# Kernel tuning notes

Measured on AMD Instinct MI355X. Metric: run time of the kernel, lower is better.

## Reference

```python
import jax, jax.numpy as jnp
import numpy as np

B, S, H, NH = 2048, 200, 128, 4
NEG = jnp.float32(-2.0**32 + 1)

def setup_inputs() -> dict:
    key = jax.random.key(0)
    k1, k2, k3, k4, k5 = jax.random.split(key, 5)
    item_eb = jax.random.normal(k1, (B, S, H), dtype=jnp.float32)
    mask = jax.random.randint(k2, (B, S), 0, 2, dtype=jnp.int32)
    pos_emb = jax.random.normal(k3, (1, S, H), dtype=jnp.float32) * 0.02
    # nn.Linear(H, 4H, bias=False): weight [4H, H]; store transposed for x @ W
    W1 = jax.random.normal(k4, (H, 4 * H), dtype=jnp.float32) * (1.0 / np.sqrt(H))
    W2 = jax.random.normal(k5, (4 * H, NH), dtype=jnp.float32) * (1.0 / np.sqrt(4 * H))
    return {"item_eb": item_eb, "mask": mask, "pos_emb": pos_emb, "W1": W1, "W2": W2}

def reference(item_eb, mask, pos_emb, W1, W2):
    x = item_eb.reshape(-1, S, H)                       # [B,S,H]
    x_pos = x + pos_emb                                  # broadcast position add
    hidden = jnp.tanh(jnp.einsum('bsh,hf->bsf', x_pos, W1))   # [B,S,4H]
    att = jnp.einsum('bsf,fk->bks', hidden, W2)          # [B,NH,S] (transpose fused)
    att = jnp.where(mask[:, None, :] == 0, NEG, att)     # masked fill
    att = jax.nn.softmax(att, axis=-1)                   # [B,NH,S]
    interest = jnp.einsum('bks,bsh->bkh', att, x)        # [B,NH,H]
    return interest
```

## Files before the change

### kernel.cpp

```cpp
#include <hip/hip_runtime.h>
#include <hip/hip_bf16.h>

typedef _Float16 half8 __attribute__((ext_vector_type(8)));
typedef _Float16 half4 __attribute__((ext_vector_type(4)));
typedef float f32x4 __attribute__((ext_vector_type(4)));

#define SS 200
#define HH 128
#define NHD 4
#define FH 512
#define NTILES 32
#define MTILES 13
#define RW 144
#define NEGF (-4294967295.0f)

__global__ void swizzle_w1(const float* __restrict__ W1, _Float16* __restrict__ dst) {
    int tid = blockIdx.x * blockDim.x + threadIdx.x;
    int j    = tid & 7;
    int lane = (tid >> 3) & 63;
    int ks   = (tid >> 9) & 3;
    int nt   = tid >> 11;
    int k = ks * 32 + (lane >> 4) * 8 + j;
    int n = nt * 16 + (lane & 15);
    dst[tid] = (_Float16)W1[k * FH + n];
}

__device__ __forceinline__ float tanh_fast(float x) {
    x = fminf(fmaxf(x, -15.0f), 15.0f);
    float e = __expf(x + x);
    return (e - 1.0f) * __builtin_amdgcn_rcpf(e + 1.0f);
}

__device__ __forceinline__ f32x4 mfma16(half8 a, half8 b, f32x4 c) {
    return __builtin_amdgcn_mfma_f32_16x16x32_f16(a, b, c, 0, 0, 0);
}

template<int USE_WS>
__global__ __launch_bounds__(256, USE_WS ? 4 : 1)
void mhan_main(const float* __restrict__ item, const int* __restrict__ mask,
               const float* __restrict__ pos, const float* __restrict__ W1,
               const float* __restrict__ W2, const _Float16* __restrict__ w1sw,
               float* __restrict__ out)
{
    __shared__ __align__(16) _Float16 xs[16 * RW];
    __shared__ float4 w2s[FH];
    __shared__ float  attw[208 * NHD];
    __shared__ half8  w1s_lds[USE_WS ? 1 : (NTILES * 4 * 64)];

    int tid = threadIdx.x;
    int b   = blockIdx.x;
    int lane = tid & 63, wave = tid >> 6;
    int q = lane >> 4, c = lane & 15;

    int rowslot[4], colslot[4];
    {
        half8 pc_, pone;
#pragma unroll
        for (int j = 0; j < 8; ++j) { pc_[j] = (_Float16)(float)c; pone[j] = (_Float16)0.03125f; }
        f32x4 z = {0.f,0.f,0.f,0.f};
        f32x4 pr = mfma16(pc_, pone, z);
        f32x4 pcv = mfma16(pone, pc_, z);
#pragma unroll
        for (int r = 0; r < 4; ++r) {
            int rv = (int)(pr[r] + 0.5f);
            int cv = (int)(pcv[r] + 0.5f);
            rowslot[r] = rv < 0 ? 0 : (rv > 15 ? 15 : rv);
            colslot[r] = cv < 0 ? 0 : (cv > 15 ? 15 : cv);
        }
    }
    int okA = 1, okB = 1;
#pragma unroll
    for (int r = 0; r < 4; ++r) {
        okA &= (rowslot[r] == q * 4 + r) & (colslot[r] == c);
        okB &= (rowslot[r] == c) & (colslot[r] == q * 4 + r);
    }
    int path = __all(okA) ? 0 : (__all(okB) ? 1 : 2);

    if constexpr (!USE_WS) {
        _Float16* w1f = (_Float16*)w1s_lds;
        for (int idx = tid; idx < HH * FH; idx += 256) {
            int j = idx & 7; int ln = (idx >> 3) & 63;
            int ks = (idx >> 9) & 3; int nt = idx >> 11;
            int k = ks * 32 + (ln >> 4) * 8 + j;
            int n = nt * 16 + (ln & 15);
            w1f[idx] = (_Float16)W1[k * FH + n];
        }
    }
    for (int i = tid; i < FH; i += 256) w2s[i] = ((const float4*)W2)[i];
    for (int i = tid; i < 208 * NHD; i += 256) attw[i] = 0.0f;
    __syncthreads();

    const half8* w1p;
    if constexpr (USE_WS) w1p = (const half8*)w1sw;
    else                  w1p = w1s_lds;

    const float* xb = item + (size_t)b * SS * HH;
    int nt0 = wave * 8;

#pragma unroll 1
    for (int mt = 0; mt < MTILES; ++mt) {
#pragma unroll
        for (int i = 0; i < 2; ++i) {
            int u = tid + i * 256;
            int row = u >> 5, col4 = u & 31;
            int grow = mt * 16 + row;
            float4 xv = make_float4(0.f,0.f,0.f,0.f), pv = xv;
            if (grow < SS) {
                xv = ((const float4*)(xb + grow * HH))[col4];
                pv = ((const float4*)(pos + grow * HH))[col4];
            }
            half4 h;
            h[0] = (_Float16)(xv.x + pv.x); h[1] = (_Float16)(xv.y + pv.y);
            h[2] = (_Float16)(xv.z + pv.z); h[3] = (_Float16)(xv.w + pv.w);
            *(half4*)&xs[row * RW + col4 * 4] = h;
        }
        __syncthreads();

        half8 af[4];
        {
            const _Float16* xp = &xs[c * RW + q * 8];
#pragma unroll
            for (int ks = 0; ks < 4; ++ks) af[ks] = *(const half8*)(xp + ks * 32);
        }

        float attp[4][NHD];
#pragma unroll
        for (int r = 0; r < 4; ++r)
#pragma unroll
            for (int k = 0; k < NHD; ++k) attp[r][k] = 0.0f;

#pragma unroll 1
        for (int nt = nt0; nt < nt0 + 8; nt += 2) {
            const half8* bp0 = &w1p[(nt * 4) * 64 + lane];
            const half8* bp1 = &w1p[((nt + 1) * 4) * 64 + lane];
            half8 bf0[4], bf1[4];
#pragma unroll
            for (int ks = 0; ks < 4; ++ks) { bf0[ks] = bp0[ks * 64]; bf1[ks] = bp1[ks * 64]; }
            f32x4 acc0 = {0.f,0.f,0.f,0.f}, acc1 = {0.f,0.f,0.f,0.f};
#pragma unroll
            for (int ks = 0; ks < 4; ++ks) {
                acc0 = mfma16(af[ks], bf0[ks], acc0);
                acc1 = mfma16(af[ks], bf1[ks], acc1);
            }
#pragma unroll
            for (int r = 0; r < 4; ++r) {
                float4 w0 = w2s[nt * 16 + colslot[r]];
                float4 w1v = w2s[(nt + 1) * 16 + colslot[r]];
                float h0 = tanh_fast(acc0[r]);
                float h1 = tanh_fast(acc1[r]);
                attp[r][0] += h0 * w0.x + h1 * w1v.x;
                attp[r][1] += h0 * w0.y + h1 * w1v.y;
                attp[r][2] += h0 * w0.z + h1 * w1v.z;
                attp[r][3] += h0 * w0.w + h1 * w1v.w;
            }
        }

        if (path == 0) {
#pragma unroll
            for (int r = 0; r < 4; ++r)
#pragma unroll
                for (int k = 0; k < NHD; ++k) {
                    float v = attp[r][k];
                    v += __shfl_xor(v, 1);
                    v += __shfl_xor(v, 2);
                    v += __shfl_xor(v, 4);
                    v += __shfl_xor(v, 8);
                    if (c == 0)
                        atomicAdd(&attw[(mt * 16 + rowslot[r]) * NHD + k], v);
                }
        } else if (path == 1) {
#pragma unroll
            for (int k = 0; k < NHD; ++k) {
                float v = attp[0][k] + attp[1][k] + attp[2][k] + attp[3][k];
                v += __shfl_xor(v, 16);
                v += __shfl_xor(v, 32);
                if (q == 0)
                    atomicAdd(&attw[(mt * 16 + c) * NHD + k], v);
            }
        } else {
#pragma unroll
            for (int r = 0; r < 4; ++r)
#pragma unroll
                for (int k = 0; k < NHD; ++k)
                    atomicAdd(&attw[(mt * 16 + rowslot[r]) * NHD + k], attp[r][k]);
        }
        __syncthreads();
    }

    {
        int k = wave;
        float l[4];
        float m = -__builtin_inff();
#pragma unroll
        for (int i = 0; i < 4; ++i) {
            int s = lane + i * 64;
            if (s < SS) {
                float lv = (mask[(size_t)b * SS + s] != 0) ? attw[s * NHD + k] : NEGF;
                l[i] = lv;
                m = fmaxf(m, lv);
            } else {
                l[i] = -__builtin_inff();
            }
        }
#pragma unroll
        for (int off = 32; off >= 1; off >>= 1) m = fmaxf(m, __shfl_xor(m, off));
        float e[4], sum = 0.0f;
#pragma unroll
        for (int i = 0; i < 4; ++i) {
            e[i] = (l[i] == -__builtin_inff()) ? 0.0f : __expf(l[i] - m);
            sum += e[i];
        }
#pragma unroll
        for (int off = 32; off >= 1; off >>= 1) sum += __shfl_xor(sum, off);
        float inv = __builtin_amdgcn_rcpf(sum);
#pragma unroll
        for (int i = 0; i < 4; ++i) {
            int s = lane + i * 64;
            if (s < SS) attw[s * NHD + k] = e[i] * inv;
        }
    }

    {
        int k = wave;
        float ax = 0.0f, ay = 0.0f;
#pragma unroll 8
        for (int s = 0; s < SS; ++s) {
            float w = attw[s * NHD + k];
            float2 xv = ((const float2*)(xb + s * HH))[lane];
            ax += w * xv.x;
            ay += w * xv.y;
        }
        size_t o = ((size_t)b * NHD + k) * HH + lane * 2;
        float2 ov; ov.x = ax; ov.y = ay;
        *(float2*)(out + o) = ov;
    }
}

extern "C" void kernel_launch(void* const* d_in, const int* in_sizes, int n_in,
                              void* d_out, int out_size, void* d_ws, size_t ws_size,
                              hipStream_t stream) {
    const float* item = (const float*)d_in[0];
    const int*   mask = (const int*)d_in[1];
    const float* pos  = (const float*)d_in[2];
    const float* W1   = (const float*)d_in[3];
    const float* W2   = (const float*)d_in[4];
    float* out = (float*)d_out;

    int B = in_sizes[0] / (SS * HH);
    int use_ws = (ws_size >= (size_t)(HH * FH * sizeof(_Float16))) ? 1 : 0;

    if (use_ws) {
        hipLaunchKernelGGL(swizzle_w1, dim3((HH * FH) / 256), dim3(256), 0, stream,
                           W1, (_Float16*)d_ws);
        mhan_main<1><<<dim3(B), dim3(256), 0, stream>>>(
            item, mask, pos, W1, W2, (const _Float16*)d_ws, out);
    } else {
        mhan_main<0><<<dim3(B), dim3(256), 0, stream>>>(
            item, mask, pos, W1, W2, (const _Float16*)nullptr, out);
    }
}
```

Baseline: 514.8 us.

## Process two 16-row M tiles per phase to reuse W1 fragments

```diff
diff --git a/kernel.cpp b/kernel.cpp
--- a/kernel.cpp
+++ b/kernel.cpp
@@ -10,7 +10,8 @@
 #define NHD 4
 #define FH 512
 #define NTILES 32
-#define MTILES 13
+#define NPHASES 7
+#define AROWS 224
 #define RW 144
 #define NEGF (-4294967295.0f)
 
@@ -36,15 +37,15 @@
 }
 
 template<int USE_WS>
-__global__ __launch_bounds__(256, USE_WS ? 4 : 1)
+__global__ __launch_bounds__(256, USE_WS ? 3 : 1)
 void mhan_main(const float* __restrict__ item, const int* __restrict__ mask,
                const float* __restrict__ pos, const float* __restrict__ W1,
                const float* __restrict__ W2, const _Float16* __restrict__ w1sw,
                float* __restrict__ out)
 {
-    __shared__ __align__(16) _Float16 xs[16 * RW];
+    __shared__ __align__(16) _Float16 xs[32 * RW];
     __shared__ float4 w2s[FH];
-    __shared__ float  attw[208 * NHD];
+    __shared__ float  attw[AROWS * NHD];
     __shared__ half8  w1s_lds[USE_WS ? 1 : (NTILES * 4 * 64)];
 
     int tid = threadIdx.x;
@@ -87,7 +88,7 @@
         }
     }
     for (int i = tid; i < FH; i += 256) w2s[i] = ((const float4*)W2)[i];
-    for (int i = tid; i < 208 * NHD; i += 256) attw[i] = 0.0f;
+    for (int i = tid; i < AROWS * NHD; i += 256) attw[i] = 0.0f;
     __syncthreads();
 
     const half8* w1p;
@@ -98,12 +99,12 @@
     int nt0 = wave * 8;
 
 #pragma unroll 1
-    for (int mt = 0; mt < MTILES; ++mt) {
-#pragma unroll
-        for (int i = 0; i < 2; ++i) {
+    for (int ph = 0; ph < NPHASES; ++ph) {
+#pragma unroll
+        for (int i = 0; i < 4; ++i) {
             int u = tid + i * 256;
             int row = u >> 5, col4 = u & 31;
-            int grow = mt * 16 + row;
+            int grow = ph * 32 + row;
             float4 xv = make_float4(0.f,0.f,0.f,0.f), pv = xv;
             if (grow < SS) {
                 xv = ((const float4*)(xb + grow * HH))[col4];
@@ -116,73 +117,117 @@
         }
         __syncthreads();
 
-        half8 af[4];
-        {
-            const _Float16* xp = &xs[c * RW + q * 8];
-#pragma unroll
-            for (int ks = 0; ks < 4; ++ks) af[ks] = *(const half8*)(xp + ks * 32);
-        }
-
-        float attp[4][NHD];
-#pragma unroll
-        for (int r = 0; r < 4; ++r)
-#pragma unroll
-            for (int k = 0; k < NHD; ++k) attp[r][k] = 0.0f;
-
-#pragma unroll 1
-        for (int nt = nt0; nt < nt0 + 8; nt += 2) {
-            const half8* bp0 = &w1p[(nt * 4) * 64 + lane];
-            const half8* bp1 = &w1p[((nt + 1) * 4) * 64 + lane];
-            half8 bf0[4], bf1[4];
-#pragma unroll
-            for (int ks = 0; ks < 4; ++ks) { bf0[ks] = bp0[ks * 64]; bf1[ks] = bp1[ks * 64]; }
-            f32x4 acc0 = {0.f,0.f,0.f,0.f}, acc1 = {0.f,0.f,0.f,0.f};
-#pragma unroll
-            for (int ks = 0; ks < 4; ++ks) {
-                acc0 = mfma16(af[ks], bf0[ks], acc0);
-                acc1 = mfma16(af[ks], bf1[ks], acc1);
-            }
-#pragma unroll
-            for (int r = 0; r < 4; ++r) {
-                float4 w0 = w2s[nt * 16 + colslot[r]];
-                float4 w1v = w2s[(nt + 1) * 16 + colslot[r]];
-                float h0 = tanh_fast(acc0[r]);
-                float h1 = tanh_fast(acc1[r]);
-                attp[r][0] += h0 * w0.x + h1 * w1v.x;
-                attp[r][1] += h0 * w0.y + h1 * w1v.y;
-                attp[r][2] += h0 * w0.z + h1 * w1v.z;
-                attp[r][3] += h0 * w0.w + h1 * w1v.w;
-            }
-        }
+        half8 af[2][4];
+#pragma unroll
+        for (int t = 0; t < 2; ++t) {
+            const _Float16* xp = &xs[(t * 16 + c) * RW + q * 8];
+#pragma unroll
+            for (int ks = 0; ks < 4; ++ks) af[t][ks] = *(const half8*)(xp + ks * 32);
+        }
+
+        float attp[2][4][NHD];
+#pragma unroll
+        for (int t = 0; t < 2; ++t)
+#pragma unroll
+            for (int r = 0; r < 4; ++r)
+#pragma unroll
+                for (int k = 0; k < NHD; ++k) attp[t][r][k] = 0.0f;
 
         if (path == 0) {
 #pragma unroll
-            for (int r = 0; r < 4; ++r)
-#pragma unroll
-                for (int k = 0; k < NHD; ++k) {
-                    float v = attp[r][k];
-                    v += __shfl_xor(v, 1);
-                    v += __shfl_xor(v, 2);
-                    v += __shfl_xor(v, 4);
-                    v += __shfl_xor(v, 8);
-                    if (c == 0)
-                        atomicAdd(&attw[(mt * 16 + rowslot[r]) * NHD + k], v);
+            for (int np = 0; np < 4; ++np) {
+                int nt = nt0 + 2 * np;
+                const half8* bp0 = &w1p[(nt * 4) * 64 + lane];
+                const half8* bp1 = &w1p[((nt + 1) * 4) * 64 + lane];
+                half8 bf0[4], bf1[4];
+#pragma unroll
+                for (int ks = 0; ks < 4; ++ks) { bf0[ks] = bp0[ks * 64]; bf1[ks] = bp1[ks * 64]; }
+                float4 w20 = w2s[nt * 16 + c];
+                float4 w21 = w2s[(nt + 1) * 16 + c];
+#pragma unroll
+                for (int t = 0; t < 2; ++t) {
+                    f32x4 acc0 = {0.f,0.f,0.f,0.f}, acc1 = {0.f,0.f,0.f,0.f};
+#pragma unroll
+                    for (int ks = 0; ks < 4; ++ks) {
+                        acc0 = mfma16(af[t][ks], bf0[ks], acc0);
+                        acc1 = mfma16(af[t][ks], bf1[ks], acc1);
+                    }
+#pragma unroll
+                    for (int r = 0; r < 4; ++r) {
+                        float h0 = tanh_fast(acc0[r]);
+                        float h1 = tanh_fast(acc1[r]);
+                        attp[t][r][0] += h0 * w20.x + h1 * w21.x;
+                        attp[t][r][1] += h0 * w20.y + h1 * w21.y;
+                        attp[t][r][2] += h0 * w20.z + h1 * w21.z;
+                        attp[t][r][3] += h0 * w20.w + h1 * w21.w;
+                    }
                 }
-        } else if (path == 1) {
-#pragma unroll
-            for (int k = 0; k < NHD; ++k) {
-                float v = attp[0][k] + attp[1][k] + attp[2][k] + attp[3][k];
-                v += __shfl_xor(v, 16);
-                v += __shfl_xor(v, 32);
-                if (q == 0)
-                    atomicAdd(&attw[(mt * 16 + c) * NHD + k], v);
-            }
+            }
+#pragma unroll
+            for (int t = 0; t < 2; ++t)
+#pragma unroll
+                for (int r = 0; r < 4; ++r)
+#pragma unroll
+                    for (int k = 0; k < NHD; ++k) {
+                        float v = attp[t][r][k];
+                        v += __shfl_xor(v, 1);
+                        v += __shfl_xor(v, 2);
+                        v += __shfl_xor(v, 4);
+                        v += __shfl_xor(v, 8);
+                        if (c == 0)
+                            atomicAdd(&attw[((ph * 2 + t) * 16 + rowslot[r]) * NHD + k], v);
+                    }
         } else {
 #pragma unroll
-            for (int r = 0; r < 4; ++r)
-#pragma unroll
-                for (int k = 0; k < NHD; ++k)
-                    atomicAdd(&attw[(mt * 16 + rowslot[r]) * NHD + k], attp[r][k]);
+            for (int np = 0; np < 4; ++np) {
+                int nt = nt0 + 2 * np;
+                const half8* bp0 = &w1p[(nt * 4) * 64 + lane];
+                const half8* bp1 = &w1p[((nt + 1) * 4) * 64 + lane];
+                half8 bf0[4], bf1[4];
+#pragma unroll
+                for (int ks = 0; ks < 4; ++ks) { bf0[ks] = bp0[ks * 64]; bf1[ks] = bp1[ks * 64]; }
+#pragma unroll
+                for (int t = 0; t < 2; ++t) {
+                    f32x4 acc0 = {0.f,0.f,0.f,0.f}, acc1 = {0.f,0.f,0.f,0.f};
+#pragma unroll
+                    for (int ks = 0; ks < 4; ++ks) {
+                        acc0 = mfma16(af[t][ks], bf0[ks], acc0);
+                        acc1 = mfma16(af[t][ks], bf1[ks], acc1);
+                    }
+#pragma unroll
+                    for (int r = 0; r < 4; ++r) {
+                        float4 w20 = w2s[nt * 16 + colslot[r]];
+                        float4 w21 = w2s[(nt + 1) * 16 + colslot[r]];
+                        float h0 = tanh_fast(acc0[r]);
+                        float h1 = tanh_fast(acc1[r]);
+                        attp[t][r][0] += h0 * w20.x + h1 * w21.x;
+                        attp[t][r][1] += h0 * w20.y + h1 * w21.y;
+                        attp[t][r][2] += h0 * w20.z + h1 * w21.z;
+                        attp[t][r][3] += h0 * w20.w + h1 * w21.w;
+                    }
+                }
+            }
+            if (path == 1) {
+#pragma unroll
+                for (int t = 0; t < 2; ++t)
+#pragma unroll
+                    for (int k = 0; k < NHD; ++k) {
+                        float v = attp[t][0][k] + attp[t][1][k] + attp[t][2][k] + attp[t][3][k];
+                        v += __shfl_xor(v, 16);
+                        v += __shfl_xor(v, 32);
+                        if (q == 0)
+                            atomicAdd(&attw[((ph * 2 + t) * 16 + c) * NHD + k], v);
+                    }
+            } else {
+#pragma unroll
+                for (int t = 0; t < 2; ++t)
+#pragma unroll
+                    for (int r = 0; r < 4; ++r)
+#pragma unroll
+                        for (int k = 0; k < NHD; ++k)
+                            atomicAdd(&attw[((ph * 2 + t) * 16 + rowslot[r]) * NHD + k],
+                                      attp[t][r][k]);
+            }
         }
         __syncthreads();
     }
```

Result: slower. 655.8 us (+27.4%).
